# Optimization experiments

Hardware: AMD Instinct MI355X
Metric: run time of the kernel (lower is better)

## Reference

```python
import math
import jax, jax.numpy as jnp
import numpy as np

B, L, D = 8, 2048, 1024
NEG_INF = 1e9  # config.INF stand-in; large finite value keeps fully-masked rows NaN-free


def setup_inputs() -> dict:
    key = jax.random.key(0)
    k1, k2, k3, k4, k5, k6 = jax.random.split(key, 6)
    s = 1.0 / math.sqrt(D)
    return {
        "input_seq": jax.random.normal(k1, (B, L, D), dtype=jnp.float32),
        "input_lens": jax.random.randint(k2, (B,), 1, L + 1, dtype=jnp.int64),
        "output_seq": jax.random.normal(k3, (B, L, D), dtype=jnp.float32),
        "Wk": jax.random.normal(k4, (D, D), dtype=jnp.float32) * s,
        "Wv": jax.random.normal(k5, (D, D), dtype=jnp.float32) * s,
        "Wq": jax.random.normal(k6, (D, D), dtype=jnp.float32) * s,
    }


def reference(input_seq, input_lens, output_seq, Wk, Wv, Wq):
    # Linear(embed_dim, embed_dim, bias=False): y = x @ W^T
    k = jnp.einsum('bld,ed->ble', input_seq, Wk)   # [B, L, D]
    v = jnp.einsum('bld,ed->ble', input_seq, Wv)   # [B, L, D]
    q = jnp.einsum('bld,ed->ble', output_seq, Wq)  # [B, L, D]

    scores = jnp.einsum('bqd,bkd->bqk', q, k) / math.sqrt(D)  # [B, Lq, Lk]

    # Faithful to the torch code (apply_mask=True): mask [B, L] is unsqueezed
    # on the LAST dim -> [B, L, 1], so it broadcasts over the KEY axis and
    # effectively masks query rows with index >= input_lens.
    valid = jnp.arange(L)[None, :] < input_lens[:, None]      # [B, L]
    scores = jnp.where(valid[:, :, None], scores, -NEG_INF)

    attn = jax.nn.softmax(scores, axis=-1)                    # [B, Lq, Lk]
    # dropout is identity in eval mode (deterministic reference)
    context = jnp.einsum('bqk,bkd->bqd', attn, v)             # [B, Lq, D]
    return context, attn
```

## Files before the change

### kernel.cpp

```cpp
#include <hip/hip_runtime.h>
#include <hip/hip_bf16.h>

#define B_ 8
#define L_ 2048
#define D_ 1024
#define CTX_ELEMS (B_ * L_ * D_)

typedef __bf16 bf16x8 __attribute__((ext_vector_type(8)));
typedef float f32x4 __attribute__((ext_vector_type(4)));
typedef unsigned short u16x8 __attribute__((ext_vector_type(8)));
typedef unsigned short u16x4 __attribute__((ext_vector_type(4)));

typedef __attribute__((address_space(1))) void GV;
typedef __attribute__((address_space(3))) void LV;
#define GLL16(g, l) __builtin_amdgcn_global_load_lds((GV*)(g), (LV*)(l), 16, 0, 0)

__device__ __forceinline__ unsigned short f2bf(float f) {
    union { float f; unsigned u; } c; c.f = f;
    unsigned u = c.u;
    u += 0x7fffu + ((u >> 16) & 1u);
    return (unsigned short)(u >> 16);
}

__global__ __launch_bounds__(256) void cvt_kernel(
    const float* __restrict__ x, const float* __restrict__ y,
    const float* __restrict__ Wk, const float* __restrict__ Wv,
    const float* __restrict__ Wq,
    unsigned short* __restrict__ xb, unsigned short* __restrict__ yb,
    unsigned short* __restrict__ wkb, unsigned short* __restrict__ wvb,
    unsigned short* __restrict__ wqb)
{
    const float* src; unsigned short* dst; int n4;
    switch (blockIdx.y) {
        case 0:  src = x;  dst = xb;  n4 = CTX_ELEMS / 4; break;
        case 1:  src = y;  dst = yb;  n4 = CTX_ELEMS / 4; break;
        case 2:  src = Wk; dst = wkb; n4 = D_ * D_ / 4;   break;
        case 3:  src = Wv; dst = wvb; n4 = D_ * D_ / 4;   break;
        default: src = Wq; dst = wqb; n4 = D_ * D_ / 4;   break;
    }
    const int stride = gridDim.x * 256;
    for (int i = blockIdx.x * 256 + threadIdx.x; i < n4; i += stride) {
        float4 f = ((const float4*)src)[i];
        u16x4 o = { f2bf(f.x), f2bf(f.y), f2bf(f.z), f2bf(f.w) };
        ((u16x4*)dst)[i] = o;
    }
}

#define GEMM_VARS                                              \
    const int tid = threadIdx.x;                               \
    const int wave = tid >> 6, lane = tid & 63;                \
    const int wr = wave >> 1, wc = wave & 1;                   \
    const int lrow = lane & 15, quad = lane >> 4;              \
    const int gr = lane >> 2, gc = (lane & 3) * 8;

#define GEMM_KLOOP(Ag, lda, Bg, ldb, K)                                        \
    for (int k0 = 0; k0 < (K); k0 += 32) {                                     \
        __syncthreads();                                                       \
        _Pragma("unroll")                                                      \
        for (int r = 0; r < 2; r++) {                                          \
            const int seg = wave * 2 + r;                                      \
            GLL16((Ag) + (size_t)(m0 + seg * 16 + gr) * (lda) + k0 + gc,       \
                  sA + seg * 512);                                             \
            GLL16((Bg) + (size_t)(n0 + seg * 16 + gr) * (ldb) + k0 + gc,       \
                  sB + seg * 512);                                             \
        }                                                                      \
        __syncthreads();                                                       \
        bf16x8 av[4], bv[4];                                                   \
        _Pragma("unroll")                                                      \
        for (int i = 0; i < 4; i++)                                            \
            av[i] = *(const bf16x8*)&sA[(wr * 64 + i * 16 + lrow) * 32 + quad * 8]; \
        _Pragma("unroll")                                                      \
        for (int j = 0; j < 4; j++)                                            \
            bv[j] = *(const bf16x8*)&sB[(wc * 64 + j * 16 + lrow) * 32 + quad * 8]; \
        _Pragma("unroll")                                                      \
        for (int i = 0; i < 4; i++)                                            \
            _Pragma("unroll")                                                  \
            for (int j = 0; j < 4; j++)                                        \
                acc[i][j] = __builtin_amdgcn_mfma_f32_16x16x32_bf16(           \
                    av[i], bv[j], acc[i][j], 0, 0, 0);                         \
    }

__global__ __launch_bounds__(256) void proj_kernel(
    const unsigned short* __restrict__ xb, const unsigned short* __restrict__ yb,
    const unsigned short* __restrict__ wkb, const unsigned short* __restrict__ wvb,
    const unsigned short* __restrict__ wqb,
    unsigned short* __restrict__ kb, unsigned short* __restrict__ qb,
    unsigned short* __restrict__ vtb)
{
    __shared__ unsigned short smem[128 * 136];
    unsigned short* sA = smem;
    unsigned short* sB = smem + 4096;

    const unsigned short* Ag; const unsigned short* Bg;
    const int z = blockIdx.z;
    if (z == 0)      { Ag = xb; Bg = wkb; }
    else if (z == 1) { Ag = xb; Bg = wvb; }
    else             { Ag = yb; Bg = wqb; }

    const int m0 = blockIdx.x * 128;
    const int n0 = blockIdx.y * 128;
    GEMM_VARS

    f32x4 acc[4][4];
#pragma unroll
    for (int i = 0; i < 4; i++)
#pragma unroll
        for (int j = 0; j < 4; j++) acc[i][j] = (f32x4){0.f, 0.f, 0.f, 0.f};

    GEMM_KLOOP(Ag, D_, Bg, D_, D_)

    if (z != 1) {
        unsigned short* out = (z == 0) ? kb : qb;
#pragma unroll
        for (int i = 0; i < 4; i++) {
            const int m = m0 + wr * 64 + i * 16 + quad * 4;
#pragma unroll
            for (int j = 0; j < 4; j++) {
                const int n = n0 + wc * 64 + j * 16 + lrow;
#pragma unroll
                for (int r = 0; r < 4; r++)
                    out[(size_t)(m + r) * D_ + n] = f2bf(acc[i][j][r]);
            }
        }
    } else {
        __syncthreads();
#pragma unroll
        for (int i = 0; i < 4; i++) {
            const int m = wr * 64 + i * 16 + quad * 4;
#pragma unroll
            for (int j = 0; j < 4; j++) {
                const int n = wc * 64 + j * 16 + lrow;
#pragma unroll
                for (int r = 0; r < 4; r++)
                    smem[n * 136 + m + r] = f2bf(acc[i][j][r]);
            }
        }
        __syncthreads();
        const int b  = m0 >> 11;
        const int l0 = m0 & 2047;
        unsigned short* vt = vtb + (size_t)b * D_ * L_ + l0;
#pragma unroll
        for (int it = 0; it < 8; it++) {
            const int idx = it * 256 + tid;
            const int n  = idx >> 4;
            const int c8 = (idx & 15) * 8;
            u16x8 val = *(const u16x8*)&smem[n * 136 + c8];
            *(u16x8*)&vt[(size_t)(n0 + n) * L_ + c8] = val;
        }
    }
}

__global__ __launch_bounds__(256) void scores_kernel(
    const unsigned short* __restrict__ qb, const unsigned short* __restrict__ kb,
    float* __restrict__ attn)
{
    __shared__ unsigned short sA[4096];
    __shared__ unsigned short sB[4096];
    const int bz = blockIdx.z;
    const unsigned short* Ag = qb + (size_t)bz * L_ * D_;
    const unsigned short* Bg = kb + (size_t)bz * L_ * D_;
    float* out = attn + (size_t)bz * L_ * L_;

    const int m0 = blockIdx.x * 128;
    const int n0 = blockIdx.y * 128;
    GEMM_VARS

    f32x4 acc[4][4];
#pragma unroll
    for (int i = 0; i < 4; i++)
#pragma unroll
        for (int j = 0; j < 4; j++) acc[i][j] = (f32x4){0.f, 0.f, 0.f, 0.f};

    GEMM_KLOOP(Ag, D_, Bg, D_, D_)

#pragma unroll
    for (int i = 0; i < 4; i++) {
        const int m = m0 + wr * 64 + i * 16 + quad * 4;
#pragma unroll
        for (int j = 0; j < 4; j++) {
            const int n = n0 + wc * 64 + j * 16 + lrow;
#pragma unroll
            for (int r = 0; r < 4; r++)
                out[(size_t)(m + r) * L_ + n] = acc[i][j][r] * 0.03125f;
        }
    }
}

__global__ __launch_bounds__(256) void softmax_kernel(
    float* __restrict__ attn, const int* __restrict__ lens,
    unsigned short* __restrict__ attn_bf)
{
    const int r  = blockIdx.x;
    const int b  = r >> 11;
    const int qi = r & 2047;
    float* rowp = attn + (size_t)r * L_;
    unsigned short* rowb = attn_bf + (size_t)r * L_;
    const int tid = threadIdx.x;

    if (qi >= lens[b]) {
        const float u = 1.0f / 2048.0f;
        const unsigned short ub = f2bf(u);
#pragma unroll
        for (int j = 0; j < 8; j++) {
            rowp[j * 256 + tid] = u;
            rowb[j * 256 + tid] = ub;
        }
        return;
    }

    float v[8];
#pragma unroll
    for (int j = 0; j < 8; j++) v[j] = rowp[j * 256 + tid];

    float m = v[0];
#pragma unroll
    for (int j = 1; j < 8; j++) m = fmaxf(m, v[j]);
#pragma unroll
    for (int off = 32; off > 0; off >>= 1) m = fmaxf(m, __shfl_xor(m, off, 64));

    __shared__ float redm[4];
    __shared__ float reds[4];
    const int wave = tid >> 6, lane = tid & 63;
    if (lane == 0) redm[wave] = m;
    __syncthreads();
    m = fmaxf(fmaxf(redm[0], redm[1]), fmaxf(redm[2], redm[3]));

    float s = 0.f;
#pragma unroll
    for (int j = 0; j < 8; j++) { v[j] = __expf(v[j] - m); s += v[j]; }
#pragma unroll
    for (int off = 32; off > 0; off >>= 1) s += __shfl_xor(s, off, 64);
    if (lane == 0) reds[wave] = s;
    __syncthreads();
    s = reds[0] + reds[1] + reds[2] + reds[3];

    const float inv = 1.0f / s;
#pragma unroll
    for (int j = 0; j < 8; j++) {
        const float p = v[j] * inv;
        rowp[j * 256 + tid] = p;
        rowb[j * 256 + tid] = f2bf(p);
    }
}

__global__ __launch_bounds__(256) void context_kernel(
    const unsigned short* __restrict__ attn_bf, const unsigned short* __restrict__ vtb,
    float* __restrict__ ctx)
{
    __shared__ unsigned short sA[4096];
    __shared__ unsigned short sB[4096];
    const int bz = blockIdx.z;
    const unsigned short* Ag = attn_bf + (size_t)bz * L_ * L_;
    const unsigned short* Bg = vtb + (size_t)bz * D_ * L_;
    float* out = ctx + (size_t)bz * L_ * D_;

    const int m0 = blockIdx.x * 128;
    const int n0 = blockIdx.y * 128;
    GEMM_VARS

    f32x4 acc[4][4];
#pragma unroll
    for (int i = 0; i < 4; i++)
#pragma unroll
        for (int j = 0; j < 4; j++) acc[i][j] = (f32x4){0.f, 0.f, 0.f, 0.f};

    GEMM_KLOOP(Ag, L_, Bg, L_, L_)

#pragma unroll
    for (int i = 0; i < 4; i++) {
        const int m = m0 + wr * 64 + i * 16 + quad * 4;
#pragma unroll
        for (int j = 0; j < 4; j++) {
            const int n = n0 + wc * 64 + j * 16 + lrow;
#pragma unroll
            for (int r = 0; r < 4; r++)
                out[(size_t)(m + r) * D_ + n] = acc[i][j][r];
        }
    }
}

extern "C" void kernel_launch(void* const* d_in, const int* in_sizes, int n_in,
                              void* d_out, int out_size, void* d_ws, size_t ws_size,
                              hipStream_t stream) {
    const float* x    = (const float*)d_in[0];
    const int*   lens = (const int*)d_in[1];
    const float* y    = (const float*)d_in[2];
    const float* Wk   = (const float*)d_in[3];
    const float* Wv   = (const float*)d_in[4];
    const float* Wq   = (const float*)d_in[5];

    float* ctx  = (float*)d_out;
    float* attn = (float*)d_out + CTX_ELEMS;

    unsigned short* kb      = (unsigned short*)d_ws;
    unsigned short* qb      = kb + CTX_ELEMS;
    unsigned short* vtb     = qb + CTX_ELEMS;
    unsigned short* attn_bf = (unsigned short*)d_ws;

    unsigned short* xb  = (unsigned short*)attn;
    unsigned short* yb  = xb + CTX_ELEMS;
    unsigned short* wkb = yb + CTX_ELEMS;
    unsigned short* wvb = wkb + D_ * D_;
    unsigned short* wqb = wvb + D_ * D_;

    cvt_kernel<<<dim3(2048, 5), 256, 0, stream>>>(x, y, Wk, Wv, Wq,
                                                  xb, yb, wkb, wvb, wqb);
    proj_kernel<<<dim3(128, 8, 3), 256, 0, stream>>>(xb, yb, wkb, wvb, wqb,
                                                     kb, qb, vtb);
    scores_kernel<<<dim3(16, 16, B_), 256, 0, stream>>>(qb, kb, attn);
    softmax_kernel<<<dim3(B_ * L_), 256, 0, stream>>>(attn, lens, attn_bf);
    context_kernel<<<dim3(16, 8, B_), 256, 0, stream>>>(attn_bf, vtb, ctx);
}
```

Baseline: 655.6 us.

## Swizzle GEMM tile order, compute V transposed directly, vectorize softmax

Blocks in the projection, scores and context GEMMs are remapped from a 2D grid to a linear index laid out in 4x4 groups, so neighbouring workgroups share A/B tiles in L2. The V projection swaps operands (Wv times x) so it produces V^T directly, and all projections now write their output through LDS in two halves with coalesced 16-byte stores. The softmax kernel uses float4 loads and stores and 4-wide bf16 stores. The extra LDS staging adds syncs to the projection epilogue.

```diff
diff --git a/kernel.cpp b/kernel.cpp
--- a/kernel.cpp
+++ b/kernel.cpp
@@ -87,18 +87,21 @@
     unsigned short* __restrict__ kb, unsigned short* __restrict__ qb,
     unsigned short* __restrict__ vtb)
 {
-    __shared__ unsigned short smem[128 * 136];
+    __shared__ unsigned short smem[8192];
     unsigned short* sA = smem;
     unsigned short* sB = smem + 4096;
 
-    const unsigned short* Ag; const unsigned short* Bg;
     const int z = blockIdx.z;
-    if (z == 0)      { Ag = xb; Bg = wkb; }
-    else if (z == 1) { Ag = xb; Bg = wvb; }
-    else             { Ag = yb; Bg = wqb; }
-
-    const int m0 = blockIdx.x * 128;
-    const int n0 = blockIdx.y * 128;
+    const int lin = blockIdx.x;
+    const int sq = lin >> 4, w = lin & 15;
+    const int big = (sq & 31) * 4 + (w & 3);
+    const int sml = (sq >> 5) * 4 + (w >> 2);
+    int m0, n0;
+    const unsigned short *Ag, *Bg;
+    if (z == 0)      { Ag = xb;  Bg = wkb; m0 = big * 128; n0 = sml * 128; }
+    else if (z == 1) { Ag = wvb; Bg = xb;  m0 = sml * 128; n0 = big * 128; }
+    else             { Ag = yb;  Bg = wqb; m0 = big * 128; n0 = sml * 128; }
+
     GEMM_VARS
 
     f32x4 acc[4][4];
@@ -109,43 +112,36 @@
 
     GEMM_KLOOP(Ag, D_, Bg, D_, D_)
 
-    if (z != 1) {
-        unsigned short* out = (z == 0) ? kb : qb;
-#pragma unroll
-        for (int i = 0; i < 4; i++) {
-            const int m = m0 + wr * 64 + i * 16 + quad * 4;
-#pragma unroll
-            for (int j = 0; j < 4; j++) {
-                const int n = n0 + wc * 64 + j * 16 + lrow;
-#pragma unroll
-                for (int r = 0; r < 4; r++)
-                    out[(size_t)(m + r) * D_ + n] = f2bf(acc[i][j][r]);
-            }
-        }
+    unsigned short* base; size_t ostride;
+    if (z == 1) {
+        base = vtb + (size_t)(n0 >> 11) * D_ * L_ + (size_t)m0 * L_ + (n0 & 2047);
+        ostride = L_;
     } else {
+        base = ((z == 0) ? kb : qb) + (size_t)m0 * D_ + n0;
+        ostride = D_;
+    }
+
+#pragma unroll
+    for (int h = 0; h < 2; h++) {
         __syncthreads();
-#pragma unroll
-        for (int i = 0; i < 4; i++) {
-            const int m = wr * 64 + i * 16 + quad * 4;
-#pragma unroll
-            for (int j = 0; j < 4; j++) {
-                const int n = wc * 64 + j * 16 + lrow;
-#pragma unroll
-                for (int r = 0; r < 4; r++)
-                    smem[n * 136 + m + r] = f2bf(acc[i][j][r]);
-            }
+        if (wr == h) {
+#pragma unroll
+            for (int i = 0; i < 4; i++)
+#pragma unroll
+                for (int j = 0; j < 4; j++)
+#pragma unroll
+                    for (int r = 0; r < 4; r++)
+                        smem[(i * 16 + quad * 4 + r) * 128 + wc * 64 + j * 16 + lrow]
+                            = f2bf(acc[i][j][r]);
         }
         __syncthreads();
-        const int b  = m0 >> 11;
-        const int l0 = m0 & 2047;
-        unsigned short* vt = vtb + (size_t)b * D_ * L_ + l0;
-#pragma unroll
-        for (int it = 0; it < 8; it++) {
-            const int idx = it * 256 + tid;
-            const int n  = idx >> 4;
-            const int c8 = (idx & 15) * 8;
-            u16x8 val = *(const u16x8*)&smem[n * 136 + c8];
-            *(u16x8*)&vt[(size_t)(n0 + n) * L_ + c8] = val;
+#pragma unroll
+        for (int c = 0; c < 4; c++) {
+            const int idx = c * 256 + tid;
+            const int rr  = idx >> 4;
+            const int c8  = (idx & 15) * 8;
+            *(u16x8*)(base + (size_t)(h * 64 + rr) * ostride + c8)
+                = *(const u16x8*)&smem[rr * 128 + c8];
         }
     }
 }
@@ -154,15 +150,20 @@
     const unsigned short* __restrict__ qb, const unsigned short* __restrict__ kb,
     float* __restrict__ attn)
 {
-    __shared__ unsigned short sA[4096];
-    __shared__ unsigned short sB[4096];
+    __shared__ unsigned short smem[8192];
+    unsigned short* sA = smem;
+    unsigned short* sB = smem + 4096;
+
     const int bz = blockIdx.z;
     const unsigned short* Ag = qb + (size_t)bz * L_ * D_;
     const unsigned short* Bg = kb + (size_t)bz * L_ * D_;
     float* out = attn + (size_t)bz * L_ * L_;
 
-    const int m0 = blockIdx.x * 128;
-    const int n0 = blockIdx.y * 128;
+    const int lin = blockIdx.x;
+    const int sq = lin >> 4, w = lin & 15;
+    const int m0 = ((sq & 3) * 4 + (w & 3)) * 128;
+    const int n0 = ((sq >> 2) * 4 + (w >> 2)) * 128;
+
     GEMM_VARS
 
     f32x4 acc[4][4];
@@ -193,28 +194,24 @@
     const int r  = blockIdx.x;
     const int b  = r >> 11;
     const int qi = r & 2047;
-    float* rowp = attn + (size_t)r * L_;
-    unsigned short* rowb = attn_bf + (size_t)r * L_;
+    float4* rowp = (float4*)(attn + (size_t)r * L_);
+    u16x4*  rowb = (u16x4*)(attn_bf + (size_t)r * L_);
     const int tid = threadIdx.x;
 
     if (qi >= lens[b]) {
         const float u = 1.0f / 2048.0f;
-        const unsigned short ub = f2bf(u);
-#pragma unroll
-        for (int j = 0; j < 8; j++) {
-            rowp[j * 256 + tid] = u;
-            rowb[j * 256 + tid] = ub;
-        }
+        const unsigned short us = f2bf(u);
+        const float4 uf = {u, u, u, u};
+        const u16x4 ub = {us, us, us, us};
+        rowp[tid] = uf; rowp[tid + 256] = uf;
+        rowb[tid] = ub; rowb[tid + 256] = ub;
         return;
     }
 
-    float v[8];
-#pragma unroll
-    for (int j = 0; j < 8; j++) v[j] = rowp[j * 256 + tid];
-
-    float m = v[0];
-#pragma unroll
-    for (int j = 1; j < 8; j++) m = fmaxf(m, v[j]);
+    float4 v0 = rowp[tid], v1 = rowp[tid + 256];
+
+    float m = fmaxf(fmaxf(fmaxf(v0.x, v0.y), fmaxf(v0.z, v0.w)),
+                    fmaxf(fmaxf(v1.x, v1.y), fmaxf(v1.z, v1.w)));
 #pragma unroll
     for (int off = 32; off > 0; off >>= 1) m = fmaxf(m, __shfl_xor(m, off, 64));
 
@@ -225,9 +222,11 @@
     __syncthreads();
     m = fmaxf(fmaxf(redm[0], redm[1]), fmaxf(redm[2], redm[3]));
 
-    float s = 0.f;
-#pragma unroll
-    for (int j = 0; j < 8; j++) { v[j] = __expf(v[j] - m); s += v[j]; }
+    v0.x = __expf(v0.x - m); v0.y = __expf(v0.y - m);
+    v0.z = __expf(v0.z - m); v0.w = __expf(v0.w - m);
+    v1.x = __expf(v1.x - m); v1.y = __expf(v1.y - m);
+    v1.z = __expf(v1.z - m); v1.w = __expf(v1.w - m);
+    float s = (v0.x + v0.y) + (v0.z + v0.w) + (v1.x + v1.y) + (v1.z + v1.w);
 #pragma unroll
     for (int off = 32; off > 0; off >>= 1) s += __shfl_xor(s, off, 64);
     if (lane == 0) reds[wave] = s;
@@ -235,27 +234,32 @@
     s = reds[0] + reds[1] + reds[2] + reds[3];
 
     const float inv = 1.0f / s;
-#pragma unroll
-    for (int j = 0; j < 8; j++) {
-        const float p = v[j] * inv;
-        rowp[j * 256 + tid] = p;
-        rowb[j * 256 + tid] = f2bf(p);
-    }
+    v0.x *= inv; v0.y *= inv; v0.z *= inv; v0.w *= inv;
+    v1.x *= inv; v1.y *= inv; v1.z *= inv; v1.w *= inv;
+    rowp[tid] = v0; rowp[tid + 256] = v1;
+    u16x4 b0 = { f2bf(v0.x), f2bf(v0.y), f2bf(v0.z), f2bf(v0.w) };
+    u16x4 b1 = { f2bf(v1.x), f2bf(v1.y), f2bf(v1.z), f2bf(v1.w) };
+    rowb[tid] = b0; rowb[tid + 256] = b1;
 }
 
 __global__ __launch_bounds__(256) void context_kernel(
     const unsigned short* __restrict__ attn_bf, const unsigned short* __restrict__ vtb,
     float* __restrict__ ctx)
 {
-    __shared__ unsigned short sA[4096];
-    __shared__ unsigned short sB[4096];
+    __shared__ unsigned short smem[8192];
+    unsigned short* sA = smem;
+    unsigned short* sB = smem + 4096;
+
     const int bz = blockIdx.z;
     const unsigned short* Ag = attn_bf + (size_t)bz * L_ * L_;
     const unsigned short* Bg = vtb + (size_t)bz * D_ * L_;
     float* out = ctx + (size_t)bz * L_ * D_;
 
-    const int m0 = blockIdx.x * 128;
-    const int n0 = blockIdx.y * 128;
+    const int lin = blockIdx.x;
+    const int sq = lin >> 4, w = lin & 15;
+    const int m0 = ((sq & 3) * 4 + (w & 3)) * 128;
+    const int n0 = ((sq >> 2) * 4 + (w >> 2)) * 128;
+
     GEMM_VARS
 
     f32x4 acc[4][4];
@@ -305,9 +309,9 @@
 
     cvt_kernel<<<dim3(2048, 5), 256, 0, stream>>>(x, y, Wk, Wv, Wq,
                                                   xb, yb, wkb, wvb, wqb);
-    proj_kernel<<<dim3(128, 8, 3), 256, 0, stream>>>(xb, yb, wkb, wvb, wqb,
-                                                     kb, qb, vtb);
-    scores_kernel<<<dim3(16, 16, B_), 256, 0, stream>>>(qb, kb, attn);
+    proj_kernel<<<dim3(1024, 1, 3), 256, 0, stream>>>(xb, yb, wkb, wvb, wqb,
+                                                      kb, qb, vtb);
+    scores_kernel<<<dim3(256, 1, B_), 256, 0, stream>>>(qb, kb, attn);
     softmax_kernel<<<dim3(B_ * L_), 256, 0, stream>>>(attn, lens, attn_bf);
-    context_kernel<<<dim3(16, 8, B_), 256, 0, stream>>>(attn_bf, vtb, ctx);
-}
+    context_kernel<<<dim3(128, 1, B_), 256, 0, stream>>>(attn_bf, vtb, ctx);
+}
```

After: 648.4 us. Within noise of the previous version (-1.1%).
